# Kernel tuning notes

Hardware: AMD Instinct MI355X
Metric: run time of the kernel (lower is better)

Reference implementation:

```python
import jax, jax.numpy as jnp
import numpy as np

K, d = 8, 8
D = K * d          # 64
B, T, N = 8, 12, 325


def _xavier(key, shape):
    fan_out, fan_in = shape
    lim = (6.0 / (fan_in + fan_out)) ** 0.5
    return jax.random.uniform(key, shape, jnp.float32, -lim, lim)


def setup_inputs() -> dict:
    key = jax.random.key(0)
    ks = jax.random.split(key, 8)
    return {
        "X": jax.random.normal(ks[0], (B, T, N, D), jnp.float32),
        "STE": jax.random.normal(ks[1], (B, T, N, D), jnp.float32),
        "adj": jax.random.randint(ks[2], (N, N), 0, 2, jnp.int32),
        "W7": _xavier(ks[3], (D, 2 * D)), "b7": jnp.zeros((D,), jnp.float32),
        "W8": _xavier(ks[4], (D, 2 * D)), "b8": jnp.zeros((D,), jnp.float32),
        "W9": _xavier(ks[5], (D, 2 * D)), "b9": jnp.zeros((D,), jnp.float32),
        "W10": _xavier(ks[6], (D, D)), "b10": jnp.zeros((D,), jnp.float32),
        "W11": _xavier(ks[7], (D, D)), "b11": jnp.zeros((D,), jnp.float32),
    }


def reference(X, STE, adj, W7, b7, W8, b8, W9, b9, W10, b10, W11, b11):
    # X, STE: [B, T, N, D]
    x = jnp.concatenate([X, STE], axis=-1)  # [B,T,N,2D]
    gelu = lambda t: jax.nn.gelu(t, approximate=False)  # torch F.gelu default = exact erf
    q = gelu(x @ W7.T + b7)  # [B,T,N,D]
    k = gelu(x @ W8.T + b8)
    v = gelu(x @ W9.T + b9)
    # split D into K heads of size d (equivalent to torch split(dim=-1)+cat(dim=0))
    heads = lambda t: t.reshape(B, T, N, K, d)
    q, k, v = heads(q), heads(k), heads(v)
    # scores: [K,B,T,N,N] == torch's [K*B,T,N,N]
    attn = jnp.einsum('btnkd,btmkd->kbtnm', q, k) / (d ** 0.5)
    attn = jnp.where(adj > 0, attn, jnp.float32(-9e15))
    attn = jax.nn.softmax(attn, axis=-1)
    out = jnp.einsum('kbtnm,btmkd->btnkd', attn, v).reshape(B, T, N, D)
    out = gelu(out @ W10.T + b10) @ W11.T + b11
    return out
```

## Files before the change

kernel.cpp:

```cpp
#include <hip/hip_runtime.h>
#include <math.h>

#define NN 325
#define BT 96
#define NROWS (BT * NN)
#define SCL (0.35355339059327373f * 1.4426950408889634f)

typedef _Float16 half_t;
typedef half_t half4_t __attribute__((ext_vector_type(4)));
typedef half_t half2_t __attribute__((ext_vector_type(2)));
typedef float float4_t __attribute__((ext_vector_type(4)));

__device__ __forceinline__ float gelu_f(float x) {
    return 0.5f * x * (1.0f + erff(x * 0.70710678118654752f));
}

__global__ void prep_kernel(const int* __restrict__ adj,
                            const float* __restrict__ W7,
                            const float* __restrict__ W8,
                            const float* __restrict__ W9,
                            const float* __restrict__ W10,
                            const float* __restrict__ W11,
                            unsigned int* __restrict__ packedT,
                            half_t* __restrict__ w789,
                            half_t* __restrict__ wab)
{
    int idx = blockIdx.x * 256 + threadIdx.x;
    if (idx < 11 * NN) {
        int w = idx / NN, n = idx - w * NN;
        unsigned int bits = 0u;
        #pragma unroll 8
        for (int j = 0; j < 32; ++j) {
            int m = w * 32 + j;
            if (m < NN && adj[n * NN + m] > 0) bits |= (1u << j);
        }
        packedT[w * NN + n] = bits;
    } else if (idx < 3575 + 24576) {
        int i = idx - 3575;
        int p = i >> 13, r = i & 8191;
        const float* Wp = (p == 0) ? W7 : (p == 1) ? W8 : W9;
        w789[i] = (half_t)Wp[r];
    } else if (idx < 3575 + 24576 + 8192) {
        int i = idx - 28151;
        int p = i >> 12, r = i & 4095;
        wab[i] = (half_t)(p ? W11[r] : W10[r]);
    }
}

#define XS 136

__device__ __forceinline__ void qkv_stage_w(const half_t* __restrict__ src,
                                            half_t* dst, int tid)
{
    #pragma unroll
    for (int idx = tid; idx < 1024; idx += 256) {
        int c = idx >> 4, g = idx & 15;
        *(uint4*)&dst[c * XS + g * 8] = *(const uint4*)&src[c * 128 + g * 8];
    }
}

__device__ __forceinline__ void qkv_compute(
    const half_t* x16, const half_t* wb, const float* __restrict__ b,
    half_t* __restrict__ outp, float oscale,
    int row0, int rbase, int ch, int l15, int quad)
{
    float4_t acc[2];
    #pragma unroll
    for (int cc = 0; cc < 2; ++cc) {
        float bias = b[(ch * 2 + cc) * 16 + l15];
        acc[cc] = (float4_t){bias, bias, bias, bias};
    }
    #pragma unroll
    for (int kk = 0; kk < 8; ++kk) {
        half4_t a = *(const half4_t*)&x16[(rbase + l15) * XS + kk * 16 + quad * 4];
        #pragma unroll
        for (int cc = 0; cc < 2; ++cc) {
            half4_t bf = *(const half4_t*)
                &wb[((ch * 2 + cc) * 16 + l15) * XS + kk * 16 + quad * 4];
            acc[cc] = __builtin_amdgcn_mfma_f32_16x16x16f16(a, bf, acc[cc], 0, 0, 0);
        }
    }
    #pragma unroll
    for (int cc = 0; cc < 2; ++cc) {
        #pragma unroll
        for (int rr = 0; rr < 4; ++rr) {
            int R = row0 + rbase + quad * 4 + rr;
            outp[R * 64 + (ch * 2 + cc) * 16 + l15] =
                (half_t)(gelu_f(acc[cc][rr]) * oscale);
        }
    }
}

__global__ __launch_bounds__(256) void qkv_kernel(
    const float* __restrict__ X, const float* __restrict__ STE,
    const half_t* __restrict__ w789,
    const float* __restrict__ b7, const float* __restrict__ b8,
    const float* __restrict__ b9,
    half_t* __restrict__ q, half_t* __restrict__ k, half_t* __restrict__ v)
{
    __shared__ __attribute__((aligned(16))) half_t x16[32 * XS];
    __shared__ __attribute__((aligned(16))) half_t wbuf[64 * XS];
    const int tid  = threadIdx.x;
    const int row0 = blockIdx.x * 32;

    #pragma unroll
    for (int idx = tid; idx < 1024; idx += 256) {
        int r = idx >> 5, c4 = idx & 31;
        int R = row0 + r;
        float4 f = (c4 < 16) ? *(const float4*)(X + (long)R * 64 + c4 * 4)
                             : *(const float4*)(STE + (long)R * 64 + (c4 - 16) * 4);
        half4_t hv;
        hv[0] = (half_t)f.x; hv[1] = (half_t)f.y;
        hv[2] = (half_t)f.z; hv[3] = (half_t)f.w;
        *(half4_t*)&x16[r * XS + c4 * 4] = hv;
    }
    qkv_stage_w(w789, wbuf, tid);
    __syncthreads();

    const int lane = tid & 63, wv = tid >> 6;
    const int l15 = lane & 15, quad = lane >> 4;
    const int rbase = (wv & 1) * 16, ch = wv >> 1;

    qkv_compute(x16, wbuf, b7, q, SCL, row0, rbase, ch, l15, quad);
    __syncthreads();
    qkv_stage_w(w789 + 8192, wbuf, tid);
    __syncthreads();
    qkv_compute(x16, wbuf, b8, k, 1.0f, row0, rbase, ch, l15, quad);
    __syncthreads();
    qkv_stage_w(w789 + 16384, wbuf, tid);
    __syncthreads();
    qkv_compute(x16, wbuf, b9, v, 1.0f, row0, rbase, ch, l15, quad);
}

__global__ __launch_bounds__(256) void attn_kernel(
    const half_t* __restrict__ q16g, const half_t* __restrict__ k16g,
    const half_t* __restrict__ v16g, const unsigned int* __restrict__ packedT,
    half_t* __restrict__ ao)
{
    __shared__ __attribute__((aligned(16))) half_t K16[336 * 20];
    __shared__ __attribute__((aligned(16))) half_t VT16[16 * 344];
    const int tid = threadIdx.x;
    const int h = blockIdx.x, bt = blockIdx.y, z = blockIdx.z;
    const long base = (long)(bt * NN) * 64 + h * 8;

    const half4_t z4 = {(half_t)0.f, (half_t)0.f, (half_t)0.f, (half_t)0.f};

    for (int idx = tid; idx < 16 * 344 / 2; idx += 256)
        ((half2_t*)VT16)[idx] = (half2_t)(half_t)0.f;
    __syncthreads();
    for (int i = tid; i < 344; i += 256)
        VT16[8 * 344 + i] = (half_t)1.0f;

    for (int r = tid; r < 336; r += 256) {
        half4_t ka = z4, kb = z4;
        if (r < NN) {
            ka = *(const half4_t*)(k16g + base + r * 64);
            kb = *(const half4_t*)(k16g + base + r * 64 + 4);
        }
        *(half4_t*)&K16[r * 20]      = ka;
        *(half4_t*)&K16[r * 20 + 4]  = kb;
        *(half4_t*)&K16[r * 20 + 8]  = z4;
        *(half4_t*)&K16[r * 20 + 12] = z4;
    }

    for (int mp = tid; mp < 168; mp += 256) {
        int m0 = 2 * mp, m1 = 2 * mp + 1;
        half4_t v0a = z4, v0b = z4, v1a = z4, v1b = z4;
        if (m0 < NN) {
            v0a = *(const half4_t*)(v16g + base + m0 * 64);
            v0b = *(const half4_t*)(v16g + base + m0 * 64 + 4);
        }
        if (m1 < NN) {
            v1a = *(const half4_t*)(v16g + base + m1 * 64);
            v1b = *(const half4_t*)(v16g + base + m1 * 64 + 4);
        }
        #pragma unroll
        for (int c = 0; c < 4; ++c) {
            half2_t p0; p0[0] = v0a[c]; p0[1] = v1a[c];
            half2_t p1; p1[0] = v0b[c]; p1[1] = v1b[c];
            *(half2_t*)&VT16[c * 344 + 2 * mp]       = p0;
            *(half2_t*)&VT16[(c + 4) * 344 + 2 * mp] = p1;
        }
    }
    __syncthreads();

    const int lane = tid & 63;
    const int wv   = tid >> 6;
    const int l15  = lane & 15;
    const int quad = lane >> 4;
    const int qsh  = quad * 4;

    for (int t = z * 7 + wv; t < z * 7 + 7; t += 4) {
        const int n  = t * 16 + l15;
        const int nq = (n < NN) ? n : (NN - 1);

        half4_t qf = z4;
        if (quad < 2)
            qf = *(const half4_t*)(q16g + base + (long)nq * 64 + qsh);

        float rm = 0.0f;
        #pragma unroll
        for (int mt = 0; mt < 21; ++mt) {
            half4_t kf = *(const half4_t*)&K16[(mt * 16 + l15) * 20 + qsh];
            float4_t s = __builtin_amdgcn_mfma_f32_16x16x16f16(
                kf, qf, (float4_t){0.f, 0.f, 0.f, 0.f}, 0, 0, 0);
            rm = fmaxf(rm, fmaxf(fmaxf(s[0], s[1]), fmaxf(s[2], s[3])));
        }
        rm = fmaxf(rm, __shfl_xor(rm, 16, 64));
        rm = fmaxf(rm, __shfl_xor(rm, 32, 64));

        unsigned int mb[11];
        #pragma unroll
        for (int w = 0; w < 11; ++w) mb[w] = packedT[w * NN + nq];

        const float4_t cinit = {-rm, -rm, -rm, -rm};
        float4_t acc = {0.f, 0.f, 0.f, 0.f};
        #pragma unroll
        for (int mt = 0; mt < 21; ++mt) {
            half4_t kf = *(const half4_t*)&K16[(mt * 16 + l15) * 20 + qsh];
            float4_t s = __builtin_amdgcn_mfma_f32_16x16x16f16(
                kf, qf, cinit, 0, 0, 0);
            unsigned int sh = mb[mt >> 1] >> (((mt & 1) << 4) + qsh);
            float p0 = (sh & 1u) ? __builtin_amdgcn_exp2f(s[0]) : 0.f;
            float p1 = (sh & 2u) ? __builtin_amdgcn_exp2f(s[1]) : 0.f;
            float p2 = (sh & 4u) ? __builtin_amdgcn_exp2f(s[2]) : 0.f;
            float p3 = (sh & 8u) ? __builtin_amdgcn_exp2f(s[3]) : 0.f;
            half4_t pf;
            pf[0] = (half_t)p0; pf[1] = (half_t)p1;
            pf[2] = (half_t)p2; pf[3] = (half_t)p3;
            half4_t vf = *(const half4_t*)&VT16[l15 * 344 + mt * 16 + qsh];
            acc = __builtin_amdgcn_mfma_f32_16x16x16f16(vf, pf, acc, 0, 0, 0);
        }

        float sum = __shfl(acc[0], 32 + l15, 64);

        if (quad < 2 && n < NN) {
            float inv = 1.0f / sum;
            half4_t o;
            o[0] = (half_t)(acc[0] * inv); o[1] = (half_t)(acc[1] * inv);
            o[2] = (half_t)(acc[2] * inv); o[3] = (half_t)(acc[3] * inv);
            *(half4_t*)(ao + base + (long)n * 64 + qsh) = o;
        }
    }
}

#define PS 72

__global__ __launch_bounds__(256) void proj_kernel(
    const half_t* __restrict__ ao, const half_t* __restrict__ wab,
    const float* __restrict__ b10, const float* __restrict__ b11,
    float* __restrict__ out)
{
    __shared__ __attribute__((aligned(16))) half_t a16[32 * PS];
    __shared__ __attribute__((aligned(16))) half_t h16[32 * PS];
    __shared__ __attribute__((aligned(16))) half_t wA[64 * PS];
    __shared__ __attribute__((aligned(16))) half_t wB[64 * PS];
    const int tid  = threadIdx.x;
    const int row0 = blockIdx.x * 32;

    #pragma unroll
    for (int idx = tid; idx < 256; idx += 256) {
        int r = idx >> 3, c8 = idx & 7;
        *(uint4*)&a16[r * PS + c8 * 8] =
            *(const uint4*)(ao + (long)(row0 + r) * 64 + c8 * 8);
    }
    #pragma unroll
    for (int idx = tid; idx < 512; idx += 256) {
        int r = idx >> 3, c8 = idx & 7;
        *(uint4*)&wA[r * PS + c8 * 8] = *(const uint4*)&wab[r * 64 + c8 * 8];
        *(uint4*)&wB[r * PS + c8 * 8] = *(const uint4*)&wab[4096 + r * 64 + c8 * 8];
    }
    __syncthreads();

    const int lane = tid & 63, wv = tid >> 6;
    const int l15 = lane & 15, quad = lane >> 4;
    const int rbase = (wv & 1) * 16, ch = wv >> 1;

    float4_t acc[2];
    #pragma unroll
    for (int cc = 0; cc < 2; ++cc) {
        float bias = b10[(ch * 2 + cc) * 16 + l15];
        acc[cc] = (float4_t){bias, bias, bias, bias};
    }
    #pragma unroll
    for (int kk = 0; kk < 4; ++kk) {
        half4_t a = *(const half4_t*)&a16[(rbase + l15) * PS + kk * 16 + quad * 4];
        #pragma unroll
        for (int cc = 0; cc < 2; ++cc) {
            half4_t bf = *(const half4_t*)
                &wA[((ch * 2 + cc) * 16 + l15) * PS + kk * 16 + quad * 4];
            acc[cc] = __builtin_amdgcn_mfma_f32_16x16x16f16(a, bf, acc[cc], 0, 0, 0);
        }
    }
    #pragma unroll
    for (int cc = 0; cc < 2; ++cc) {
        #pragma unroll
        for (int rr = 0; rr < 4; ++rr)
            h16[(rbase + quad * 4 + rr) * PS + (ch * 2 + cc) * 16 + l15] =
                (half_t)gelu_f(acc[cc][rr]);
    }
    __syncthreads();

    #pragma unroll
    for (int cc = 0; cc < 2; ++cc) {
        float bias = b11[(ch * 2 + cc) * 16 + l15];
        acc[cc] = (float4_t){bias, bias, bias, bias};
    }
    #pragma unroll
    for (int kk = 0; kk < 4; ++kk) {
        half4_t a = *(const half4_t*)&h16[(rbase + l15) * PS + kk * 16 + quad * 4];
        #pragma unroll
        for (int cc = 0; cc < 2; ++cc) {
            half4_t bf = *(const half4_t*)
                &wB[((ch * 2 + cc) * 16 + l15) * PS + kk * 16 + quad * 4];
            acc[cc] = __builtin_amdgcn_mfma_f32_16x16x16f16(a, bf, acc[cc], 0, 0, 0);
        }
    }
    #pragma unroll
    for (int cc = 0; cc < 2; ++cc) {
        #pragma unroll
        for (int rr = 0; rr < 4; ++rr) {
            int R = row0 + rbase + quad * 4 + rr;
            out[R * 64 + (ch * 2 + cc) * 16 + l15] = acc[cc][rr];
        }
    }
}

extern "C" void kernel_launch(void* const* d_in, const int* in_sizes, int n_in,
                              void* d_out, int out_size, void* d_ws, size_t ws_size,
                              hipStream_t stream) {
    const float* X   = (const float*)d_in[0];
    const float* STE = (const float*)d_in[1];
    const int*   adj = (const int*)d_in[2];
    const float* W7  = (const float*)d_in[3];
    const float* b7  = (const float*)d_in[4];
    const float* W8  = (const float*)d_in[5];
    const float* b8  = (const float*)d_in[6];
    const float* W9  = (const float*)d_in[7];
    const float* b9  = (const float*)d_in[8];
    const float* W10 = (const float*)d_in[9];
    const float* b10 = (const float*)d_in[10];
    const float* W11 = (const float*)d_in[11];
    const float* b11 = (const float*)d_in[12];

    char* wsb = (char*)d_ws;
    const long S = (long)NROWS * 64;
    half_t* qb = (half_t*)wsb;
    half_t* kb = qb + S;
    half_t* vb = qb + 2 * S;
    half_t* ab = qb + 3 * S;
    unsigned int* pk = (unsigned int*)(wsb + 4 * S * sizeof(half_t));
    half_t* w789 = (half_t*)(wsb + 4 * S * sizeof(half_t) + 16384);
    half_t* wab  = w789 + 24576;

    prep_kernel<<<142, 256, 0, stream>>>(adj, W7, W8, W9, W10, W11,
                                         pk, w789, wab);
    qkv_kernel<<<dim3(975), 256, 0, stream>>>(
        X, STE, w789, b7, b8, b9, qb, kb, vb);
    attn_kernel<<<dim3(8, BT, 3), 256, 0, stream>>>(qb, kb, vb, pk, ab);
    proj_kernel<<<dim3(975), 256, 0, stream>>>(
        ab, wab, b10, b11, (float*)d_out);
}
```

Before: 162.6 us.

## Stage all QKV weights at once and merge attention z-split blocks

The QKV kernel now loads all three weight matrices into shared memory in one pass and keeps the input A-fragments in registers, so the four barriers between projections go away and each wave computes six 16-column tiles. Shared memory per block grows to about 61 KB, which can lower occupancy. The attention kernel drops its 3-way z split of query tiles, so each block handles all 21 tiles and loads K/V into shared memory once instead of three times, at the cost of fewer blocks (768). The score loops are now partially unrolled by 7 instead of fully.

```diff
diff --git a/kernel.cpp b/kernel.cpp
--- a/kernel.cpp
+++ b/kernel.cpp
@@ -49,48 +49,6 @@
 
 #define XS 136
 
-__device__ __forceinline__ void qkv_stage_w(const half_t* __restrict__ src,
-                                            half_t* dst, int tid)
-{
-    #pragma unroll
-    for (int idx = tid; idx < 1024; idx += 256) {
-        int c = idx >> 4, g = idx & 15;
-        *(uint4*)&dst[c * XS + g * 8] = *(const uint4*)&src[c * 128 + g * 8];
-    }
-}
-
-__device__ __forceinline__ void qkv_compute(
-    const half_t* x16, const half_t* wb, const float* __restrict__ b,
-    half_t* __restrict__ outp, float oscale,
-    int row0, int rbase, int ch, int l15, int quad)
-{
-    float4_t acc[2];
-    #pragma unroll
-    for (int cc = 0; cc < 2; ++cc) {
-        float bias = b[(ch * 2 + cc) * 16 + l15];
-        acc[cc] = (float4_t){bias, bias, bias, bias};
-    }
-    #pragma unroll
-    for (int kk = 0; kk < 8; ++kk) {
-        half4_t a = *(const half4_t*)&x16[(rbase + l15) * XS + kk * 16 + quad * 4];
-        #pragma unroll
-        for (int cc = 0; cc < 2; ++cc) {
-            half4_t bf = *(const half4_t*)
-                &wb[((ch * 2 + cc) * 16 + l15) * XS + kk * 16 + quad * 4];
-            acc[cc] = __builtin_amdgcn_mfma_f32_16x16x16f16(a, bf, acc[cc], 0, 0, 0);
-        }
-    }
-    #pragma unroll
-    for (int cc = 0; cc < 2; ++cc) {
-        #pragma unroll
-        for (int rr = 0; rr < 4; ++rr) {
-            int R = row0 + rbase + quad * 4 + rr;
-            outp[R * 64 + (ch * 2 + cc) * 16 + l15] =
-                (half_t)(gelu_f(acc[cc][rr]) * oscale);
-        }
-    }
-}
-
 __global__ __launch_bounds__(256) void qkv_kernel(
     const float* __restrict__ X, const float* __restrict__ STE,
     const half_t* __restrict__ w789,
@@ -99,7 +57,7 @@
     half_t* __restrict__ q, half_t* __restrict__ k, half_t* __restrict__ v)
 {
     __shared__ __attribute__((aligned(16))) half_t x16[32 * XS];
-    __shared__ __attribute__((aligned(16))) half_t wbuf[64 * XS];
+    __shared__ __attribute__((aligned(16))) half_t w16[192 * XS];
     const int tid  = threadIdx.x;
     const int row0 = blockIdx.x * 32;
 
@@ -114,22 +72,46 @@
         hv[2] = (half_t)f.z; hv[3] = (half_t)f.w;
         *(half4_t*)&x16[r * XS + c4 * 4] = hv;
     }
-    qkv_stage_w(w789, wbuf, tid);
+    #pragma unroll
+    for (int idx = tid; idx < 3072; idx += 256) {
+        int c = idx >> 4, g = idx & 15;
+        *(uint4*)&w16[c * XS + g * 8] = *(const uint4*)&w789[c * 128 + g * 8];
+    }
     __syncthreads();
 
     const int lane = tid & 63, wv = tid >> 6;
     const int l15 = lane & 15, quad = lane >> 4;
-    const int rbase = (wv & 1) * 16, ch = wv >> 1;
-
-    qkv_compute(x16, wbuf, b7, q, SCL, row0, rbase, ch, l15, quad);
-    __syncthreads();
-    qkv_stage_w(w789 + 8192, wbuf, tid);
-    __syncthreads();
-    qkv_compute(x16, wbuf, b8, k, 1.0f, row0, rbase, ch, l15, quad);
-    __syncthreads();
-    qkv_stage_w(w789 + 16384, wbuf, tid);
-    __syncthreads();
-    qkv_compute(x16, wbuf, b9, v, 1.0f, row0, rbase, ch, l15, quad);
+    const int rbase = (wv & 1) * 16;
+    const int chalf = wv >> 1;
+
+    half4_t af[8];
+    #pragma unroll
+    for (int kk = 0; kk < 8; ++kk)
+        af[kk] = *(const half4_t*)&x16[(rbase + l15) * XS + kk * 16 + quad * 4];
+
+    #pragma unroll
+    for (int ct = 0; ct < 6; ++ct) {
+        const int gcol = chalf * 96 + ct * 16;
+        const int mat  = gcol >> 6;
+        const int lc   = gcol & 63;
+        const float* bb = (mat == 0) ? b7 : (mat == 1) ? b8 : b9;
+        half_t* outp    = (mat == 0) ? q  : (mat == 1) ? k  : v;
+        const float osc = (mat == 0) ? SCL : 1.0f;
+
+        float bias = bb[lc + l15];
+        float4_t acc = (float4_t){bias, bias, bias, bias};
+        #pragma unroll
+        for (int kk = 0; kk < 8; ++kk) {
+            half4_t bf = *(const half4_t*)
+                &w16[(gcol + l15) * XS + kk * 16 + quad * 4];
+            acc = __builtin_amdgcn_mfma_f32_16x16x16f16(af[kk], bf, acc, 0, 0, 0);
+        }
+        #pragma unroll
+        for (int rr = 0; rr < 4; ++rr) {
+            int R = row0 + rbase + quad * 4 + rr;
+            outp[(long)R * 64 + lc + l15] = (half_t)(gelu_f(acc[rr]) * osc);
+        }
+    }
 }
 
 __global__ __launch_bounds__(256) void attn_kernel(
@@ -140,7 +122,7 @@
     __shared__ __attribute__((aligned(16))) half_t K16[336 * 20];
     __shared__ __attribute__((aligned(16))) half_t VT16[16 * 344];
     const int tid = threadIdx.x;
-    const int h = blockIdx.x, bt = blockIdx.y, z = blockIdx.z;
+    const int h = blockIdx.x, bt = blockIdx.y;
     const long base = (long)(bt * NN) * 64 + h * 8;
 
     const half4_t z4 = {(half_t)0.f, (half_t)0.f, (half_t)0.f, (half_t)0.f};
@@ -190,7 +172,7 @@
     const int quad = lane >> 4;
     const int qsh  = quad * 4;
 
-    for (int t = z * 7 + wv; t < z * 7 + 7; t += 4) {
+    for (int t = wv; t < 21; t += 4) {
         const int n  = t * 16 + l15;
         const int nq = (n < NN) ? n : (NN - 1);
 
@@ -199,7 +181,7 @@
             qf = *(const half4_t*)(q16g + base + (long)nq * 64 + qsh);
 
         float rm = 0.0f;
-        #pragma unroll
+        #pragma unroll 7
         for (int mt = 0; mt < 21; ++mt) {
             half4_t kf = *(const half4_t*)&K16[(mt * 16 + l15) * 20 + qsh];
             float4_t s = __builtin_amdgcn_mfma_f32_16x16x16f16(
@@ -215,7 +197,7 @@
 
         const float4_t cinit = {-rm, -rm, -rm, -rm};
         float4_t acc = {0.f, 0.f, 0.f, 0.f};
-        #pragma unroll
+        #pragma unroll 7
         for (int mt = 0; mt < 21; ++mt) {
             half4_t kf = *(const half4_t*)&K16[(mt * 16 + l15) * 20 + qsh];
             float4_t s = __builtin_amdgcn_mfma_f32_16x16x16f16(
@@ -357,7 +339,7 @@
                                          pk, w789, wab);
     qkv_kernel<<<dim3(975), 256, 0, stream>>>(
         X, STE, w789, b7, b8, b9, qb, kb, vb);
-    attn_kernel<<<dim3(8, BT, 3), 256, 0, stream>>>(qb, kb, vb, pk, ab);
+    attn_kernel<<<dim3(8, BT), 256, 0, stream>>>(qb, kb, vb, pk, ab);
     proj_kernel<<<dim3(975), 256, 0, stream>>>(
         ab, wab, b10, b11, (float*)d_out);
 }
```

Result: no change. 165.6 us (+1.8%).
